# Kernel tuning notes

Measured on AMD Instinct MI355X. Metric: run time of the kernel, lower is better.

The kernel has to match this reference:

```python
import jax, jax.numpy as jnp
import numpy as np

B, C, H, W = 16, 512, 64, 64
HEADS = 8
DIL = 2  # dilation of the 3x3 depthwise conv (padding == dilation -> shape preserving)


def setup_inputs() -> dict:
    key = jax.random.key(0)
    ks = jax.random.split(key, 4)
    x = jax.random.normal(ks[0], (B, C, H, W), jnp.float32)
    # kaiming-normal-ish scales (fan_out, relu)
    w_qkv = jax.random.normal(ks[1], (3 * C, C), jnp.float32) * (2.0 / C) ** 0.5  # 1x1 conv weight
    w_dw = jax.random.normal(ks[2], (C, 3, 3), jnp.float32) * (2.0 / 9.0) ** 0.5  # depthwise 3x3
    w_out = jax.random.normal(ks[3], (C, C), jnp.float32) * (2.0 / C) ** 0.5      # 1x1 conv weight
    temperature = jnp.sqrt(jnp.asarray(C // HEADS, jnp.float32))                  # init sqrt(dim_per_head)
    return {"x": x, "w_qkv": w_qkv, "w_dw": w_dw, "w_out": w_out, "temperature": temperature}


def _dw_conv(y, w_dw):
    # depthwise dilated 3x3 conv, padding=dilation -> same spatial size
    rhs = w_dw[:, None, :, :]  # [C,1,3,3]
    return jax.lax.conv_general_dilated(
        y, rhs, window_strides=(1, 1), padding=((DIL, DIL), (DIL, DIL)),
        rhs_dilation=(DIL, DIL), feature_group_count=y.shape[1],
        dimension_numbers=("NCHW", "OIHW", "NCHW"))


def reference(x, w_qkv, w_dw, w_out, temperature):
    b, c, h, w = x.shape
    n = h * w
    d = c // HEADS
    # 1x1 qkv projection (bias-free conv == einsum)
    qkv = jnp.einsum("oc,bchw->bohw", w_qkv, x)  # [B,3C,H,W]
    q, k, v = jnp.split(qkv, 3, axis=1)
    # same depthwise conv applied to q,k,v: fold into batch, conv once
    qkv3 = _dw_conv(jnp.concatenate([q, k, v], axis=0), w_dw)  # [3B,C,H,W]
    q, k, v = jnp.split(qkv3, 3, axis=0)
    q = q.reshape(b, HEADS, d, n)
    k = k.reshape(b, HEADS, d, n)
    v = v.reshape(b, HEADS, d, n)
    # L2 normalize along the per-head channel dim (dim=2), eps=1e-12 like F.normalize
    l2 = lambda t: t / jnp.maximum(jnp.linalg.norm(t, axis=2, keepdims=True), 1e-12)
    q = l2(q)
    k = l2(k)
    # cross-covariance attention: [B,heads,d,d]
    attn = jnp.einsum("bhdn,bhen->bhde", q, k) / jnp.maximum(temperature, 1e-5)
    attn = jax.nn.softmax(attn, axis=-1)
    # dropout is identity in eval mode
    out = jnp.einsum("bhde,bhen->bhdn", attn, v).reshape(b, c, h, w)
    return jnp.einsum("oc,bchw->bohw", w_out, out)
```

## Files before the change

kernel.cpp:

```cpp
#include <hip/hip_runtime.h>

typedef __attribute__((ext_vector_type(8))) short bf16x8;
typedef __attribute__((ext_vector_type(8))) unsigned short ushort8;
typedef __attribute__((ext_vector_type(4))) float f32x4;
typedef __attribute__((ext_vector_type(4))) unsigned int u32x4;
typedef __attribute__((ext_vector_type(2))) unsigned int u32x2;

__device__ __forceinline__ float bf2f(unsigned short u) {
  union { unsigned int i; float f; } v; v.i = ((unsigned int)u) << 16; return v.f;
}
__device__ __forceinline__ float asf(unsigned int u) {
  union { unsigned int i; float f; } v; v.i = u; return v.f;
}
__device__ __forceinline__ unsigned short f2bf(float f) {
  union { float f; unsigned int i; } v; v.f = f;
  unsigned int u = v.i;
  return (unsigned short)((u + 0x7FFFu + ((u >> 16) & 1u)) >> 16);
}
__device__ __forceinline__ void gload16(const void* g, void* l) {
  __builtin_amdgcn_global_load_lds(
      (const __attribute__((address_space(1))) void*)g,
      (__attribute__((address_space(3))) void*)l, 16, 0, 0);
}

__global__ __launch_bounds__(256) void cvt_f32_bf16(const float* __restrict__ s,
                                                    unsigned short* __restrict__ d, int n) {
  int i = blockIdx.x * 256 + threadIdx.x;
  if (i < n) d[i] = f2bf(s[i]);
}

__global__ __launch_bounds__(256) void transpose_x(const float* __restrict__ x,
                                                   unsigned short* __restrict__ xt) {
  __shared__ float tile[64][65];
  const int b = blockIdx.z, ct = blockIdx.y, nt = blockIdx.x;
  const int t = threadIdx.x;
  const int r0 = t >> 6, col = t & 63;
  const float* src = x + ((size_t)b * 512 + ct * 64) * 4096 + nt * 64;
#pragma unroll
  for (int i = 0; i < 16; ++i) {
    int r = i * 4 + r0;
    tile[r][col] = src[(size_t)r * 4096 + col];
  }
  __syncthreads();
  unsigned short* dst = xt + ((size_t)b * 4096 + nt * 64) * 512 + ct * 64;
#pragma unroll
  for (int i = 0; i < 16; ++i) {
    int n = i * 4 + r0;
    dst[(size_t)n * 512 + col] = f2bf(tile[col][n]);
  }
}

template <bool BF16OUT>
__global__ __launch_bounds__(256) void gemm_bt(const unsigned short* __restrict__ A,
                                               const unsigned short* __restrict__ B,
                                               void* __restrict__ Cv, int K, int ldc,
                                               size_t sA, size_t sB, size_t sC) {
  __shared__ unsigned short lA[2][128 * 32];
  __shared__ unsigned short lB[2][128 * 32];
  const int gx = gridDim.x, gy = gridDim.y;
  const int nwg = gx * gy * gridDim.z;
  int flat = blockIdx.x + gx * (blockIdx.y + gy * blockIdx.z);
  flat = (flat & 7) * (nwg >> 3) + (flat >> 3);
  const int bx = flat % gx;
  const int rem = flat / gx;
  const int by = rem % gy;
  const int bz = rem / gy;

  const int t = threadIdx.x;
  const int lane = t & 63;
  const int wv = t >> 6, wr = wv >> 1, wc = wv & 1;
  const size_t m0 = (size_t)by * 128;
  const size_t n0 = (size_t)bx * 128;
  A += (size_t)bz * sA;
  B += (size_t)bz * sB;
  const unsigned short* ga = A + (m0 + (t >> 2)) * (size_t)K + (t & 3) * 8;
  const unsigned short* gb = B + (n0 + (t >> 2)) * (size_t)K + (t & 3) * 8;
  const size_t gstep = (size_t)64 * K;

  f32x4 acc[4][4] = {};

  auto stage = [&](int kt, int bbuf) {
    const unsigned short* pa = ga + kt * 32;
    const unsigned short* pb = gb + kt * 32;
    char* da = (char*)(&lA[bbuf][0]) + t * 16;
    char* db = (char*)(&lB[bbuf][0]) + t * 16;
    gload16(pa, da);
    gload16(pa + gstep, da + 4096);
    gload16(pb, db);
    gload16(pb + gstep, db + 4096);
  };

  const int nk = K >> 5;
  stage(0, 0);
  __syncthreads();
  int buf = 0;
  for (int kt = 0; kt < nk; ++kt) {
    if (kt + 1 < nk) stage(kt + 1, buf ^ 1);
    const unsigned short* pa = &lA[buf][0];
    const unsigned short* pb = &lB[buf][0];
    const int ro = lane & 15, ko = (lane >> 4) * 8;
    bf16x8 af[4], bv[4];
#pragma unroll
    for (int i = 0; i < 4; ++i) af[i] = *(const bf16x8*)&pa[(wr * 64 + i * 16 + ro) * 32 + ko];
#pragma unroll
    for (int i = 0; i < 4; ++i) bv[i] = *(const bf16x8*)&pb[(wc * 64 + i * 16 + ro) * 32 + ko];
#pragma unroll
    for (int i = 0; i < 4; ++i)
#pragma unroll
      for (int j = 0; j < 4; ++j)
        acc[i][j] = __builtin_amdgcn_mfma_f32_16x16x32_bf16(af[i], bv[j], acc[i][j], 0, 0, 0);
    __syncthreads();
    buf ^= 1;
  }

  if constexpr (BF16OUT) {
    unsigned short* C = (unsigned short*)Cv + (size_t)bz * sC;
#pragma unroll
    for (int i = 0; i < 4; ++i)
#pragma unroll
      for (int j = 0; j < 4; ++j)
#pragma unroll
        for (int r = 0; r < 4; ++r) {
          size_t row = m0 + wr * 64 + i * 16 + ((lane >> 4) << 2) + r;
          size_t col = n0 + wc * 64 + j * 16 + (lane & 15);
          C[row * (size_t)ldc + col] = f2bf(acc[i][j][r]);
        }
  } else {
    float* C = (float*)Cv + (size_t)bz * sC;
#pragma unroll
    for (int i = 0; i < 4; ++i)
#pragma unroll
      for (int j = 0; j < 4; ++j)
#pragma unroll
        for (int r = 0; r < 4; ++r) {
          size_t row = m0 + wr * 64 + i * 16 + ((lane >> 4) << 2) + r;
          size_t col = n0 + wc * 64 + j * 16 + (lane & 15);
          C[row * (size_t)ldc + col] = acc[i][j][r];
        }
  }
}

struct Row3h { u32x2 v[3]; };

__global__ __launch_bounds__(256) void dwconv_norm(const unsigned short* __restrict__ Y,
                                                   const float* __restrict__ wdw,
                                                   unsigned short* __restrict__ Qb,
                                                   unsigned short* __restrict__ Kb,
                                                   unsigned short* __restrict__ Vb) {
  const int t = threadIdx.x, lane = t & 63, wv = t >> 6;
  const int bid = blockIdx.x;
  const int lbid = (bid & 7) * 768 + (bid >> 3);
  const int wid = lbid * 4 + wv;
  const int sub = wid & 7;
  const int x = (wid >> 3) & 63;
  const int grp = wid >> 9;
  const int par = sub >> 2, chhalf = (sub >> 1) & 1, half = sub & 1;
  const int b = grp / 3, part = grp - b * 3;
  const int c0 = chhalf * 256 + (lane >> 4) * 64 + (lane & 15) * 4;

  float wr[36];
  const float* wp = wdw + c0 * 9;
#pragma unroll
  for (int i = 0; i < 9; ++i) {
    f32x4 q = *(const f32x4*)(wp + i * 4);
    wr[i * 4 + 0] = q[0]; wr[i * 4 + 1] = q[1];
    wr[i * 4 + 2] = q[2]; wr[i * 4 + 3] = q[3];
  }

  const size_t ybase = (size_t)b * 4096 * 1536 + part * 512 + c0;
  const bool okm = (x >= 2), okp = (x <= 61);
  const int xm = okm ? x - 2 : x;
  const int xp = okp ? x + 2 : x;

  auto loadrow = [&](int yy) -> Row3h {
    Row3h r;
    const bool oky = ((unsigned)yy < 64u);
    const int yyc = oky ? yy : 0;
    const size_t rb = ybase + (size_t)(yyc * 64) * 1536;
    u32x2 a = *(const u32x2*)(Y + rb + (size_t)xm * 1536);
    u32x2 c = *(const u32x2*)(Y + rb + (size_t)x * 1536);
    u32x2 d = *(const u32x2*)(Y + rb + (size_t)xp * 1536);
    r.v[0] = a & ((oky && okm) ? 0xFFFFFFFFu : 0u);
    r.v[1] = c & (oky ? 0xFFFFFFFFu : 0u);
    r.v[2] = d & ((oky && okp) ? 0xFFFFFFFFu : 0u);
    return r;
  };

  const int y0 = par + half * 32;
  Row3h W[3];
  W[0] = loadrow(y0 - 2);
  W[1] = loadrow(y0);
  W[2] = loadrow(y0 + 2);

  unsigned short* dst0 = (part == 0 ? Qb : (part == 1 ? Kb : Vb)) +
                         ((size_t)b * 4096 + x) * 512 + c0;

#pragma unroll
  for (int i = 0; i < 16; ++i) {
    const int y = y0 + 2 * i;
    float acc[4] = {0.f, 0.f, 0.f, 0.f};
#pragma unroll
    for (int r = 0; r < 3; ++r) {
      const Row3h& R = W[(i + r) % 3];
#pragma unroll
      for (int xt = 0; xt < 3; ++xt) {
        const int tap = r * 3 + xt;
        const u32x2 v = R.v[xt];
#pragma unroll
        for (int m = 0; m < 2; ++m) {
          const unsigned int w2 = v[m];
          acc[2 * m]     += asf(w2 << 16)         * wr[(2 * m) * 9 + tap];
          acc[2 * m + 1] += asf(w2 & 0xFFFF0000u) * wr[(2 * m + 1) * 9 + tap];
        }
      }
    }
    if (part < 2) {
      float ss = 0.f;
#pragma unroll
      for (int j = 0; j < 4; ++j) ss += acc[j] * acc[j];
      ss += __shfl_xor(ss, 1);
      ss += __shfl_xor(ss, 2);
      ss += __shfl_xor(ss, 4);
      ss += __shfl_xor(ss, 8);
      const float rcp = 1.f / fmaxf(sqrtf(ss), 1e-12f);
#pragma unroll
      for (int j = 0; j < 4; ++j) acc[j] *= rcp;
    }
    u32x2 pk;
    pk[0] = (unsigned int)f2bf(acc[0]) | ((unsigned int)f2bf(acc[1]) << 16);
    pk[1] = (unsigned int)f2bf(acc[2]) | ((unsigned int)f2bf(acc[3]) << 16);
    *(u32x2*)(dst0 + (size_t)y * 64 * 512) = pk;
    if (i < 15) W[i % 3] = loadrow(y + 4);
  }
}

__global__ __launch_bounds__(256) void attn_partial(const unsigned short* __restrict__ Qb,
                                                    const unsigned short* __restrict__ Kb,
                                                    float* __restrict__ Spart) {
  __shared__ unsigned short sQ[4][64][72];
  __shared__ unsigned short sK[4][64][72];
  const int t = threadIdx.x, lane = t & 63, wv = t >> 6;
  const int bh = blockIdx.x >> 2;
  const int s = (blockIdx.x & 3) * 4 + wv;
  const int b = bh >> 3, h = bh & 7;
  const unsigned short* qbase = Qb + ((size_t)b * 4096) * 512 + h * 64;
  const unsigned short* kbase = Kb + ((size_t)b * 4096) * 512 + h * 64;
  f32x4 acc[4][4] = {};
  for (int ch = 0; ch < 4; ++ch) {
    const int n0 = s * 256 + ch * 64;
    const unsigned short* qp = qbase + (size_t)(n0 + lane) * 512;
    const unsigned short* kp = kbase + (size_t)(n0 + lane) * 512;
    ushort8 qv[8], kv[8];
#pragma unroll
    for (int v = 0; v < 8; ++v) qv[v] = *(const ushort8*)(qp + v * 8);
#pragma unroll
    for (int v = 0; v < 8; ++v) kv[v] = *(const ushort8*)(kp + v * 8);
#pragma unroll
    for (int v = 0; v < 8; ++v)
#pragma unroll
      for (int j = 0; j < 8; ++j) {
        sQ[wv][v * 8 + j][lane] = qv[v][j];
        sK[wv][v * 8 + j][lane] = kv[v][j];
      }
    __syncthreads();
    const int ro = lane & 15, ko = (lane >> 4) * 8;
#pragma unroll
    for (int ks = 0; ks < 2; ++ks) {
      bf16x8 af[4], bv[4];
#pragma unroll
      for (int i = 0; i < 4; ++i) af[i] = *(const bf16x8*)&sQ[wv][i * 16 + ro][ks * 32 + ko];
#pragma unroll
      for (int i = 0; i < 4; ++i) bv[i] = *(const bf16x8*)&sK[wv][i * 16 + ro][ks * 32 + ko];
#pragma unroll
      for (int i = 0; i < 4; ++i)
#pragma unroll
        for (int j = 0; j < 4; ++j)
          acc[i][j] = __builtin_amdgcn_mfma_f32_16x16x32_bf16(af[i], bv[j], acc[i][j], 0, 0, 0);
    }
    __syncthreads();
  }
  float* dst = Spart + ((size_t)bh * 16 + s) * 4096;
#pragma unroll
  for (int i = 0; i < 4; ++i)
#pragma unroll
    for (int j = 0; j < 4; ++j)
#pragma unroll
      for (int r = 0; r < 4; ++r) {
        int d = i * 16 + ((lane >> 4) << 2) + r;
        int e = j * 16 + (lane & 15);
        dst[d * 64 + e] = acc[i][j][r];
      }
}

__global__ __launch_bounds__(256) void softmax_attn(const float* __restrict__ Spart,
                                                    const float* __restrict__ tptr,
                                                    unsigned short* __restrict__ attn) {
  const int bh = blockIdx.x, t = threadIdx.x;
  const int d = t >> 2, eb = (t & 3) << 4;
  const float inv_t = 1.f / fmaxf(tptr[0], 1e-5f);
  float v[16];
#pragma unroll
  for (int i = 0; i < 16; ++i) v[i] = 0.f;
  for (int s = 0; s < 16; ++s) {
    const f32x4* p = (const f32x4*)(Spart + ((size_t)bh * 16 + s) * 4096 + d * 64 + eb);
#pragma unroll
    for (int i = 0; i < 4; ++i) {
      f32x4 q = p[i];
      v[i * 4 + 0] += q[0]; v[i * 4 + 1] += q[1];
      v[i * 4 + 2] += q[2]; v[i * 4 + 3] += q[3];
    }
  }
  float mx = -1e30f;
#pragma unroll
  for (int i = 0; i < 16; ++i) { v[i] *= inv_t; mx = fmaxf(mx, v[i]); }
  mx = fmaxf(mx, __shfl_xor(mx, 1));
  mx = fmaxf(mx, __shfl_xor(mx, 2));
  float sm = 0.f;
#pragma unroll
  for (int i = 0; i < 16; ++i) { v[i] = __expf(v[i] - mx); sm += v[i]; }
  sm += __shfl_xor(sm, 1);
  sm += __shfl_xor(sm, 2);
  const float r = 1.f / sm;
  ushort8 pk0, pk1;
#pragma unroll
  for (int i = 0; i < 8; ++i) { pk0[i] = f2bf(v[i] * r); pk1[i] = f2bf(v[8 + i] * r); }
  ushort8* dst = (ushort8*)(attn + (size_t)bh * 4096 + d * 64 + eb);
  dst[0] = pk0; dst[1] = pk1;
}

__global__ __launch_bounds__(256) void make_w2(const unsigned short* __restrict__ attn,
                                               const float* __restrict__ w_out,
                                               unsigned short* __restrict__ w2) {
  __shared__ float sA[4096];
  const int bx = blockIdx.x;
  const int bh = bx >> 1, half = bx & 1;
  const int b = bh >> 3, h = bh & 7;
  const int t = threadIdx.x;
  for (int i = t; i < 4096; i += 256) sA[i] = bf2f(attn[(size_t)bh * 4096 + i]);
  __syncthreads();
  const int o = half * 256 + t;
  float w[64];
  const float* wp = w_out + (size_t)o * 512 + h * 64;
#pragma unroll
  for (int i = 0; i < 64; i += 4) {
    f32x4 q = *(const f32x4*)(wp + i);
    w[i] = q[0]; w[i + 1] = q[1]; w[i + 2] = q[2]; w[i + 3] = q[3];
  }
  unsigned short* dst = w2 + ((size_t)b * 512 + o) * 512 + h * 64;
#pragma unroll 1
  for (int eg = 0; eg < 8; ++eg) {
    ushort8 pk;
#pragma unroll
    for (int ee = 0; ee < 8; ++ee) {
      const int e = eg * 8 + ee;
      float acc = 0.f;
#pragma unroll
      for (int dd = 0; dd < 64; ++dd) acc += w[dd] * sA[dd * 64 + e];
      pk[ee] = f2bf(acc);
    }
    *(ushort8*)(dst + eg * 8) = pk;
  }
}

extern "C" void kernel_launch(void* const* d_in, const int* in_sizes, int n_in,
                              void* d_out, int out_size, void* d_ws, size_t ws_size,
                              hipStream_t stream) {
  const float* x     = (const float*)d_in[0];
  const float* w_qkv = (const float*)d_in[1];
  const float* w_dw  = (const float*)d_in[2];
  const float* w_out = (const float*)d_in[3];
  const float* temp  = (const float*)d_in[4];
  float* out = (float*)d_out;

  char* ws = (char*)d_ws;
  const size_t MB = 1024 * 1024;
  unsigned short* Xt    = (unsigned short*)(ws);
  float*          Spart = (float*)(ws);
  unsigned short* attn  = (unsigned short*)(ws + 32 * MB);
  unsigned short* w2    = (unsigned short*)(ws + 33 * MB);
  unsigned short* Y     = (unsigned short*)(ws + 64 * MB);
  unsigned short* Qb    = (unsigned short*)(ws + 256 * MB);
  unsigned short* Kb    = (unsigned short*)(ws + 320 * MB);
  unsigned short* Vb    = (unsigned short*)(ws + 384 * MB);
  unsigned short* Wq    = (unsigned short*)(ws + 448 * MB);

  cvt_f32_bf16<<<3072, 256, 0, stream>>>(w_qkv, Wq, 1536 * 512);
  transpose_x<<<dim3(64, 8, 16), 256, 0, stream>>>(x, Xt);
  gemm_bt<true><<<dim3(12, 512, 1), 256, 0, stream>>>(Xt, Wq, Y, 512, 1536, 0, 0, 0);
  dwconv_norm<<<6144, 256, 0, stream>>>(Y, w_dw, Qb, Kb, Vb);
  attn_partial<<<512, 256, 0, stream>>>(Qb, Kb, Spart);
  softmax_attn<<<128, 256, 0, stream>>>(Spart, temp, attn);
  make_w2<<<256, 256, 0, stream>>>(attn, w_out, w2);
  gemm_bt<false><<<dim3(32, 4, 16), 256, 0, stream>>>(
      w2, Vb, out, 512, 4096,
      (size_t)512 * 512, (size_t)4096 * 512, (size_t)512 * 4096);
}
```

Before: 459.8 us.

## Use 256x256-tile QKV GEMM and give each dwconv wave a full column

Adds a dedicated QKV projection GEMM that uses 256x256 output tiles with 512 threads, a K-step of 64 and XOR-swizzled LDS staging. This replaces the generic 128-tile gemm_bt to raise operand reuse and MFMA density per LDS load. The depthwise conv kernel now has each wave walk all 32 rows of one parity instead of 16, halving the grid and the redundant halo row loads. The cost is more registers in both kernels (64 accumulator vectors per thread in the GEMM), which may reduce occupancy.

```diff
diff --git a/kernel.cpp b/kernel.cpp
--- a/kernel.cpp
+++ b/kernel.cpp
@@ -48,6 +48,88 @@
     int n = i * 4 + r0;
     dst[(size_t)n * 512 + col] = f2bf(tile[col][n]);
   }
+}
+
+__global__ __launch_bounds__(512, 2) void gemm_qkv_256(const unsigned short* __restrict__ A,
+                                                       const unsigned short* __restrict__ B,
+                                                       unsigned short* __restrict__ C) {
+  __shared__ unsigned short lA[2][256 * 64];
+  __shared__ unsigned short lB[2][256 * 64];
+  const int gx = gridDim.x;
+  const int nwg = gx * gridDim.y;
+  int flat = blockIdx.x + gx * blockIdx.y;
+  flat = (flat & 7) * (nwg >> 3) + (flat >> 3);
+  const int bx = flat % gx;
+  const int by = flat / gx;
+  const size_t m0 = (size_t)by * 256;
+  const size_t n0 = (size_t)bx * 256;
+
+  const int t = threadIdx.x;
+  const int lane = t & 63;
+  const int wid = t >> 6;
+  const int wm = wid >> 2, wn = wid & 3;
+  const int ro = lane & 15, kq = lane >> 4;
+
+  const int srow = t >> 3;
+  const int kslot = (t & 7) ^ (srow & 7);
+  const unsigned short* ga = A + (m0 + srow) * 512 + kslot * 8;
+  const unsigned short* gb = B + (n0 + srow) * 512 + kslot * 8;
+
+  f32x4 acc[8][4] = {};
+
+  auto stage = [&](int kt, int bbuf) {
+    char* da = (char*)(&lA[bbuf][0]) + t * 16;
+    char* db = (char*)(&lB[bbuf][0]) + t * 16;
+    const unsigned short* pa = ga + kt * 64;
+    const unsigned short* pb = gb + kt * 64;
+#pragma unroll
+    for (int l = 0; l < 4; ++l) {
+      gload16(pa + (size_t)(l * 64) * 512, da + l * 8192);
+      gload16(pb + (size_t)(l * 64) * 512, db + l * 8192);
+    }
+  };
+
+  stage(0, 0);
+  __syncthreads();
+  int buf = 0;
+  for (int kt = 0; kt < 8; ++kt) {
+    if (kt + 1 < 8) stage(kt + 1, buf ^ 1);
+    const unsigned short* pa = &lA[buf][0];
+    const unsigned short* pb = &lB[buf][0];
+#pragma unroll
+    for (int kk = 0; kk < 2; ++kk) {
+      const int slot = ((kk << 2) | kq) ^ (ro & 7);
+      bf16x8 a_[8], b_[4];
+#pragma unroll
+      for (int i = 0; i < 8; ++i) {
+        const int row = wm * 128 + i * 16 + ro;
+        a_[i] = *(const bf16x8*)&pa[row * 64 + slot * 8];
+      }
+#pragma unroll
+      for (int j = 0; j < 4; ++j) {
+        const int row = wn * 64 + j * 16 + ro;
+        b_[j] = *(const bf16x8*)&pb[row * 64 + slot * 8];
+      }
+#pragma unroll
+      for (int i = 0; i < 8; ++i)
+#pragma unroll
+        for (int j = 0; j < 4; ++j)
+          acc[i][j] = __builtin_amdgcn_mfma_f32_16x16x32_bf16(a_[i], b_[j], acc[i][j], 0, 0, 0);
+    }
+    __syncthreads();
+    buf ^= 1;
+  }
+
+#pragma unroll
+  for (int i = 0; i < 8; ++i)
+#pragma unroll
+    for (int j = 0; j < 4; ++j)
+#pragma unroll
+      for (int r = 0; r < 4; ++r) {
+        size_t row = m0 + wm * 128 + i * 16 + (kq << 2) + r;
+        size_t col = n0 + wn * 64 + j * 16 + ro;
+        C[row * 1536 + col] = f2bf(acc[i][j][r]);
+      }
 }
 
 template <bool BF16OUT>
@@ -149,12 +231,12 @@
                                                    unsigned short* __restrict__ Vb) {
   const int t = threadIdx.x, lane = t & 63, wv = t >> 6;
   const int bid = blockIdx.x;
-  const int lbid = (bid & 7) * 768 + (bid >> 3);
+  const int lbid = (bid & 7) * 384 + (bid >> 3);
   const int wid = lbid * 4 + wv;
-  const int sub = wid & 7;
-  const int x = (wid >> 3) & 63;
-  const int grp = wid >> 9;
-  const int par = sub >> 2, chhalf = (sub >> 1) & 1, half = sub & 1;
+  const int sub = wid & 3;
+  const int x = (wid >> 2) & 63;
+  const int grp = wid >> 8;
+  const int par = sub >> 1, chhalf = sub & 1;
   const int b = grp / 3, part = grp - b * 3;
   const int c0 = chhalf * 256 + (lane >> 4) * 64 + (lane & 15) * 4;
 
@@ -186,18 +268,18 @@
     return r;
   };
 
-  const int y0 = par + half * 32;
   Row3h W[3];
-  W[0] = loadrow(y0 - 2);
-  W[1] = loadrow(y0);
-  W[2] = loadrow(y0 + 2);
+#pragma unroll
+  for (int xt = 0; xt < 3; ++xt) W[0].v[xt] = (u32x2)(0u);
+  W[1] = loadrow(par);
+  W[2] = loadrow(par + 2);
 
   unsigned short* dst0 = (part == 0 ? Qb : (part == 1 ? Kb : Vb)) +
                          ((size_t)b * 4096 + x) * 512 + c0;
 
 #pragma unroll
-  for (int i = 0; i < 16; ++i) {
-    const int y = y0 + 2 * i;
+  for (int i = 0; i < 32; ++i) {
+    const int y = par + 2 * i;
     float acc[4] = {0.f, 0.f, 0.f, 0.f};
 #pragma unroll
     for (int r = 0; r < 3; ++r) {
@@ -230,7 +312,7 @@
     pk[0] = (unsigned int)f2bf(acc[0]) | ((unsigned int)f2bf(acc[1]) << 16);
     pk[1] = (unsigned int)f2bf(acc[2]) | ((unsigned int)f2bf(acc[3]) << 16);
     *(u32x2*)(dst0 + (size_t)y * 64 * 512) = pk;
-    if (i < 15) W[i % 3] = loadrow(y + 4);
+    if (i < 31) W[i % 3] = loadrow(y + 4);
   }
 }
 
@@ -386,8 +468,8 @@
 
   cvt_f32_bf16<<<3072, 256, 0, stream>>>(w_qkv, Wq, 1536 * 512);
   transpose_x<<<dim3(64, 8, 16), 256, 0, stream>>>(x, Xt);
-  gemm_bt<true><<<dim3(12, 512, 1), 256, 0, stream>>>(Xt, Wq, Y, 512, 1536, 0, 0, 0);
-  dwconv_norm<<<6144, 256, 0, stream>>>(Y, w_dw, Qb, Kb, Vb);
+  gemm_qkv_256<<<dim3(6, 256), 512, 0, stream>>>(Xt, Wq, Y);
+  dwconv_norm<<<3072, 256, 0, stream>>>(Y, w_dw, Qb, Kb, Vb);
   attn_partial<<<512, 256, 0, stream>>>(Qb, Kb, Spart);
   softmax_attn<<<128, 256, 0, stream>>>(Spart, temp, attn);
   make_w2<<<256, 256, 0, stream>>>(attn, w_out, w2);
```

After: 418.8 us. 1.1x faster.
